# Kernel optimization log

Measured on AMD Instinct MI355X. Metric: run time of the kernel, lower is better.

The kernel has to match this reference:

```python
import jax, jax.numpy as jnp
import numpy as np

N_DRUG = 100000
N_PROT = 100000
N_EDGE = 800000
DIM = 128


def _graph_conv(feat_src, esrc, edst, n_src, n_dst, W, b):
    """dgl GraphConv with norm='both': msg = h_src * outdeg^-1/2, sum over in-edges,
    scale by indeg^-1/2, then linear. Degrees clamped to >= 1."""
    ones = jnp.ones(esrc.shape[0], dtype=feat_src.dtype)
    deg_out = jnp.clip(jax.ops.segment_sum(ones, esrc, num_segments=n_src), 1.0)
    deg_in = jnp.clip(jax.ops.segment_sum(ones, edst, num_segments=n_dst), 1.0)
    h = feat_src * jax.lax.rsqrt(deg_out)[:, None]          # [n_src, d]
    agg = jax.ops.segment_sum(h[esrc], edst, num_segments=n_dst)  # [n_dst, d]
    agg = agg * jax.lax.rsqrt(deg_in)[:, None]
    return agg @ W + b


def _hetero_layer(hd, hp, ddi_src, ddi_dst, pdi_src, pdi_dst, ppi_src, ppi_dst, W, b):
    # relation order: 0=DDI (drug->drug), 1=PDI (protein->drug), 2=PPI (protein->protein)
    d_ddi = _graph_conv(hd, ddi_src, ddi_dst, N_DRUG, N_DRUG, W[0], b[0])
    d_pdi = _graph_conv(hp, pdi_src, pdi_dst, N_PROT, N_DRUG, W[1], b[1])
    p_ppi = _graph_conv(hp, ppi_src, ppi_dst, N_PROT, N_PROT, W[2], b[2])
    return d_ddi + d_pdi, p_ppi  # HeteroGraphConv aggregate='sum' per dst type


def setup_inputs() -> dict:
    key = jax.random.key(0)
    ks = jax.random.split(key, 16)
    s = 1.0 / np.sqrt(DIM)
    return {
        "drug_feats": jax.random.normal(ks[0], (N_DRUG, DIM), jnp.float32),
        "protein_feats": jax.random.normal(ks[1], (N_PROT, DIM), jnp.float32),
        "ddi_src": jax.random.randint(ks[2], (N_EDGE,), 0, N_DRUG),
        "ddi_dst": jax.random.randint(ks[3], (N_EDGE,), 0, N_DRUG),
        "pdi_src": jax.random.randint(ks[4], (N_EDGE,), 0, N_PROT),
        "pdi_dst": jax.random.randint(ks[5], (N_EDGE,), 0, N_DRUG),
        "ppi_src": jax.random.randint(ks[6], (N_EDGE,), 0, N_PROT),
        "ppi_dst": jax.random.randint(ks[7], (N_EDGE,), 0, N_PROT),
        "W1": jax.random.normal(ks[8], (3, DIM, DIM), jnp.float32) * s,
        "b1": jnp.zeros((3, DIM), jnp.float32),
        "W2": jax.random.normal(ks[9], (3, DIM, DIM), jnp.float32) * s,
        "b2": jnp.zeros((3, DIM), jnp.float32),
        "W3": jax.random.normal(ks[10], (3, DIM, DIM), jnp.float32) * s,
        "b3": jnp.zeros((3, DIM), jnp.float32),
    }


def reference(drug_feats, protein_feats, ddi_src, ddi_dst, pdi_src, pdi_dst,
              ppi_src, ppi_dst, W1, b1, W2, b2, W3, b3):
    e = (ddi_src, ddi_dst, pdi_src, pdi_dst, ppi_src, ppi_dst)
    hd, hp = _hetero_layer(drug_feats, protein_feats, *e, W1, b1)
    hd, hp = jax.nn.relu(hd), jax.nn.relu(hp)
    hd, hp = _hetero_layer(hd, hp, *e, W2, b2)
    hd, hp = jax.nn.relu(hd), jax.nn.relu(hp)
    hd, hp = _hetero_layer(hd, hp, *e, W3, b3)
    return hd, hp
```

## Files before the change

kernel.cpp:

```cpp
#include <hip/hip_runtime.h>
#include <hip/hip_bf16.h>
#include <stdint.h>

#define NN 100000
#define NE 800000
#define SCAN_CHUNK 2048
#define NBLK 49

#define NPART 8
#define PART_SZ ((NN + NPART - 1) / NPART)
#define KSPLIT 16
#define SEGSZ (NE / KSPLIT)
#define HBINS PART_SZ

typedef __bf16 bf16x8 __attribute__((ext_vector_type(8)));
using float4v = __attribute__((ext_vector_type(4))) float;
typedef int intv4 __attribute__((ext_vector_type(4)));
typedef unsigned short ushortv4 __attribute__((ext_vector_type(4)));

__device__ __forceinline__ float bf2f(unsigned short h) {
    unsigned int u = ((unsigned int)h) << 16;
    return __builtin_bit_cast(float, u);
}
__device__ __forceinline__ float bf_lo(unsigned int u) {
    return __builtin_bit_cast(float, u << 16);
}
__device__ __forceinline__ float bf_hi(unsigned int u) {
    return __builtin_bit_cast(float, u & 0xffff0000u);
}
__device__ __forceinline__ unsigned short f2bf(float x) {
    unsigned int u = __builtin_bit_cast(unsigned int, x);
    u += 0x7fffu + ((u >> 16) & 1u);
    return (unsigned short)(u >> 16);
}

__global__ void detect_fmt(const unsigned short* __restrict__ feat, int* __restrict__ flag) {
    __shared__ int cnt;
    if (threadIdx.x == 0) cnt = 0;
    __syncthreads();
    unsigned int u = feat[threadIdx.x];
    int e = (u >> 7) & 0xFF;
    if (e >= 90 && e <= 143) atomicAdd(&cnt, 1);
    __syncthreads();
    if (threadIdx.x == 0) {
        flag[0] = (cnt >= 160) ? 0 : 1;
        flag[1] = 0;
    }
}

__global__ __launch_bounds__(256) void convert_feats(const void* __restrict__ drug,
                                                     const void* __restrict__ prot,
                                                     unsigned short* __restrict__ hd,
                                                     unsigned short* __restrict__ hp,
                                                     const int* __restrict__ fmtp) {
    int fmt = fmtp[0];
    int i = (blockIdx.x * 256 + threadIdx.x) * 4;
    const int n1 = NN * 128;
    if (i >= 2 * n1) return;
    const void* src = (i < n1) ? drug : prot;
    unsigned short* dst = (i < n1) ? hd : hp;
    int j = (i < n1) ? i : i - n1;
    if (fmt) {
        float4 v = *(const float4*)((const float*)src + j);
        uint2 o;
        o.x = (unsigned int)f2bf(v.x) | ((unsigned int)f2bf(v.y) << 16);
        o.y = (unsigned int)f2bf(v.z) | ((unsigned int)f2bf(v.w) << 16);
        *(uint2*)(dst + j) = o;
    } else {
        *(uint2*)(dst + j) = *(const uint2*)((const unsigned short*)src + j);
    }
}

__global__ __launch_bounds__(256) void deg_hist(const int* __restrict__ s0, const int* __restrict__ d0,
                                                const int* __restrict__ s1, const int* __restrict__ d1,
                                                const int* __restrict__ s2, const int* __restrict__ d2,
                                                unsigned short* __restrict__ deg_part) {
    __shared__ unsigned int cnt[HBINS];
    int h = blockIdx.y;
    const int* a;
    switch (h) {
        case 0: a = s0; break;
        case 1: a = s1; break;
        case 2: a = s2; break;
        case 3: a = d0; break;
        case 4: a = d1; break;
        default: a = d2; break;
    }
    int part = blockIdx.x & (NPART - 1);
    int seg = blockIdx.x >> 3;
    int lo = part * HBINS;
    for (int j = threadIdx.x; j < HBINS; j += 256) cnt[j] = 0;
    __syncthreads();
    int base = seg * SEGSZ;
    int end = base + SEGSZ;
    for (int i = base + threadIdx.x * 4; i + 4 <= end; i += 1024) {
        intv4 v = *(const intv4*)(a + i);
#pragma unroll
        for (int k = 0; k < 4; k++) {
            int b = v[k] - lo;
            if ((unsigned)b < (unsigned)HBINS) atomicAdd(&cnt[b], 1u);
        }
    }
    __syncthreads();
    unsigned short* outp = deg_part + (size_t)seg * 6 * NN + (size_t)h * NN + lo;
    for (int j = threadIdx.x; j < HBINS; j += 256) outp[j] = (unsigned short)cnt[j];
}

__global__ __launch_bounds__(256) void merge_deg_rs(const unsigned short* __restrict__ deg_part,
                                                    int* __restrict__ deg_all,
                                                    float* __restrict__ rs_all) {
    int i = (blockIdx.x * 256 + threadIdx.x) * 4;
    if (i >= 6 * NN) return;
    int a0 = 0, a1 = 0, a2 = 0, a3 = 0;
#pragma unroll
    for (int s = 0; s < KSPLIT; s++) {
        ushortv4 v = *(const ushortv4*)(deg_part + (size_t)s * 6 * NN + i);
        a0 += v[0]; a1 += v[1]; a2 += v[2]; a3 += v[3];
    }
    intv4 acc; acc[0] = a0; acc[1] = a1; acc[2] = a2; acc[3] = a3;
    *(intv4*)(deg_all + i) = acc;
    float4v r;
#pragma unroll
    for (int k = 0; k < 4; k++) {
        int d = acc[k];
        if (d < 1) d = 1;
        r[k] = rsqrtf((float)d);
    }
    *(float4v*)(rs_all + i) = r;
}

__global__ __launch_bounds__(256) void scan_partial(const int* __restrict__ deg,
                                                    int* __restrict__ bsums) {
    int rel = blockIdx.y, blk = blockIdx.x;
    const int* d = deg + rel * NN;
    int base = blk * SCAN_CHUNK + threadIdx.x * 8;
    int s = 0;
#pragma unroll
    for (int i = 0; i < 8; i++) {
        int idx = base + i;
        if (idx < NN) s += d[idx];
    }
    __shared__ int wsum[4];
#pragma unroll
    for (int off = 32; off; off >>= 1) s += __shfl_down(s, off);
    if ((threadIdx.x & 63) == 0) wsum[threadIdx.x >> 6] = s;
    __syncthreads();
    if (threadIdx.x == 0) bsums[rel * NBLK + blk] = wsum[0] + wsum[1] + wsum[2] + wsum[3];
}

__global__ void scan_bsums(int* bsums) {
    int r = threadIdx.x;
    if (r < 3) {
        int run = 0;
        for (int i = 0; i < NBLK; i++) {
            int t = bsums[r * NBLK + i];
            bsums[r * NBLK + i] = run;
            run += t;
        }
    }
}

__global__ __launch_bounds__(256) void scan_final(const int* __restrict__ deg,
                                                  const int* __restrict__ bsums,
                                                  int* __restrict__ offs) {
    int rel = blockIdx.y, blk = blockIdx.x;
    const int* d = deg + rel * NN;
    int* o = offs + rel * NN;
    int base = blk * SCAN_CHUNK + threadIdx.x * 8;
    int v[8];
    int s = 0;
#pragma unroll
    for (int i = 0; i < 8; i++) {
        int idx = base + i;
        v[i] = (idx < NN) ? d[idx] : 0;
        s += v[i];
    }
    int lane = threadIdx.x & 63, wid = threadIdx.x >> 6;
    int x = s;
#pragma unroll
    for (int off = 1; off < 64; off <<= 1) {
        int t = __shfl_up(x, off);
        if (lane >= off) x += t;
    }
    __shared__ int wsum[4];
    if (lane == 63) wsum[wid] = x;
    __syncthreads();
    int woff = bsums[rel * NBLK + blk];
    for (int i = 0; i < wid; i++) woff += wsum[i];
    int run = woff + x - s;
#pragma unroll
    for (int i = 0; i < 8; i++) {
        int idx = base + i;
        if (idx < NN) {
            o[idx] = run;
            run += v[i];
        }
    }
}

__global__ __launch_bounds__(256) void seg_start_k(const unsigned short* __restrict__ deg_part,
                                                   const int* __restrict__ offs_all,
                                                   int* __restrict__ seg_start) {
    int i = blockIdx.x * 256 + threadIdx.x;
    if (i >= 3 * NN) return;
    int rel = i / NN, node = i - rel * NN;
    int run = offs_all[i];
#pragma unroll
    for (int s = 0; s < KSPLIT; s++) {
        seg_start[((size_t)s * 3 + rel) * NN + node] = run;
        run += deg_part[((size_t)s * 6 + 3 + rel) * NN + node];
    }
}

__global__ __launch_bounds__(256) void csr_fill3s(const int* __restrict__ s0, const int* __restrict__ d0,
                                                  const int* __restrict__ s1, const int* __restrict__ d1,
                                                  const int* __restrict__ s2, const int* __restrict__ d2,
                                                  const int* __restrict__ seg_start,
                                                  int* __restrict__ csr_all) {
    __shared__ int cur[PART_SZ];
    int rel = blockIdx.y;
    const int* s = (rel == 0) ? s0 : ((rel == 1) ? s1 : s2);
    const int* d = (rel == 0) ? d0 : ((rel == 1) ? d1 : d2);
    int part = blockIdx.x & (NPART - 1);
    int seg = blockIdx.x >> 3;
    int lo = part * PART_SZ;
    const int* ss = seg_start + ((size_t)seg * 3 + rel) * NN + lo;
    for (int j = threadIdx.x; j < PART_SZ; j += 256) cur[j] = ss[j];
    __syncthreads();
    int* csr = csr_all + (size_t)rel * NE;
    int base = seg * SEGSZ;
    int end = base + SEGSZ;
    for (int i = base + threadIdx.x * 4; i + 4 <= end; i += 1024) {
        intv4 dv = *(const intv4*)(d + i);
        intv4 sv = *(const intv4*)(s + i);
#pragma unroll
        for (int k = 0; k < 4; k++) {
            int b = dv[k] - lo;
            if ((unsigned)b < (unsigned)PART_SZ) {
                int pos = atomicAdd(&cur[b], 1);
                csr[pos] = sv[k];
            }
        }
    }
}

__global__ __launch_bounds__(256) void swizzle_w3(const void* __restrict__ W0,
                                                  const void* __restrict__ W1,
                                                  const void* __restrict__ W2,
                                                  int o0, int o1,
                                                  unsigned short* __restrict__ out, int lstride,
                                                  const int* __restrict__ fmtp, int ksteps) {
    int l = blockIdx.y;
    const void* W = (l == 0) ? W0 : ((l == 1) ? W1 : W2);
    int fmt = fmtp[0];
    int idx = blockIdx.x * 256 + threadIdx.x;
    int total = ksteps * 8 * 64 * 8;
    if (idx >= total) return;
    int j = idx & 7, lane = (idx >> 3) & 63, nt = (idx >> 9) & 7, ks = idx >> 12;
    int k = ks * 32 + (lane >> 4) * 8 + j;
    int n = nt * 16 + (lane & 15);
    int e = (k < 128) ? (o0 + k * 128 + n) : (o1 + (k - 128) * 128 + n);
    out[l * lstride + idx] = fmt ? f2bf(((const float*)W)[e]) : ((const unsigned short*)W)[e];
}

__global__ void bias_prep3(const void* __restrict__ b0, const void* __restrict__ b1,
                           const void* __restrict__ b2, float* __restrict__ bd,
                           float* __restrict__ bp, const int* __restrict__ fmtp) {
    int l = blockIdx.x;
    const void* b = (l == 0) ? b0 : ((l == 1) ? b1 : b2);
    int fmt = fmtp[0];
    int n = threadIdx.x;
    float v0, v1, v2;
    if (fmt) {
        const float* bf = (const float*)b;
        v0 = bf[n]; v1 = bf[128 + n]; v2 = bf[256 + n];
    } else {
        const unsigned short* bh = (const unsigned short*)b;
        v0 = bf2f(bh[n]); v1 = bf2f(bh[128 + n]); v2 = bf2f(bh[256 + n]);
    }
    bd[l * 128 + n] = v0 + v1;
    bp[l * 128 + n] = v2;
}

__device__ __forceinline__ void acc8(float* acc, uint4 v, float w) {
    acc[0] = fmaf(bf_lo(v.x), w, acc[0]);
    acc[1] = fmaf(bf_hi(v.x), w, acc[1]);
    acc[2] = fmaf(bf_lo(v.y), w, acc[2]);
    acc[3] = fmaf(bf_hi(v.y), w, acc[3]);
    acc[4] = fmaf(bf_lo(v.z), w, acc[4]);
    acc[5] = fmaf(bf_hi(v.z), w, acc[5]);
    acc[6] = fmaf(bf_lo(v.w), w, acc[6]);
    acc[7] = fmaf(bf_hi(v.w), w, acc[7]);
}

__global__ __launch_bounds__(256) void aggregate3(const unsigned short* __restrict__ hd,
                                                  const unsigned short* __restrict__ hp,
                                                  const float* __restrict__ rs_all,
                                                  const int* __restrict__ offs_all,
                                                  const int* __restrict__ deg_in_all,
                                                  const int* __restrict__ csr_all,
                                                  unsigned short* __restrict__ aggD,
                                                  unsigned short* __restrict__ aggP) {
    int rel = blockIdx.y;
    int g = blockIdx.x * 256 + threadIdx.x;
    int dst = g >> 4;
    int lane = g & 15;
    if (dst >= NN) return;
    const unsigned short* h = (rel == 0) ? hd : hp;
    const float* rs_out = rs_all + rel * NN;
    const float* rs_in = rs_all + (3 + rel) * NN;
    const int* cp = csr_all + (size_t)rel * NE + offs_all[rel * NN + dst];
    int cnt = deg_in_all[rel * NN + dst];
    unsigned short* out;
    int ostride, ocol;
    if (rel == 0)      { out = aggD; ostride = 256; ocol = 0; }
    else if (rel == 1) { out = aggD; ostride = 256; ocol = 128; }
    else               { out = aggP; ostride = 128; ocol = 0; }

    float acc[8] = {0.f, 0.f, 0.f, 0.f, 0.f, 0.f, 0.f, 0.f};
    int e = 0;
    for (; e + 4 <= cnt; e += 4) {
        int i0 = cp[e], i1 = cp[e + 1], i2 = cp[e + 2], i3 = cp[e + 3];
        float w0 = rs_out[i0], w1 = rs_out[i1], w2 = rs_out[i2], w3 = rs_out[i3];
        uint4 v0 = *(const uint4*)(h + (size_t)i0 * 128 + lane * 8);
        uint4 v1 = *(const uint4*)(h + (size_t)i1 * 128 + lane * 8);
        uint4 v2 = *(const uint4*)(h + (size_t)i2 * 128 + lane * 8);
        uint4 v3 = *(const uint4*)(h + (size_t)i3 * 128 + lane * 8);
        acc8(acc, v0, w0);
        acc8(acc, v1, w1);
        acc8(acc, v2, w2);
        acc8(acc, v3, w3);
    }
    for (; e < cnt; e++) {
        int i0 = cp[e];
        float w0 = rs_out[i0];
        uint4 v0 = *(const uint4*)(h + (size_t)i0 * 128 + lane * 8);
        acc8(acc, v0, w0);
    }
    float sc = rs_in[dst];
    uint4 o;
    o.x = (unsigned int)f2bf(acc[0] * sc) | ((unsigned int)f2bf(acc[1] * sc) << 16);
    o.y = (unsigned int)f2bf(acc[2] * sc) | ((unsigned int)f2bf(acc[3] * sc) << 16);
    o.z = (unsigned int)f2bf(acc[4] * sc) | ((unsigned int)f2bf(acc[5] * sc) << 16);
    o.w = (unsigned int)f2bf(acc[6] * sc) | ((unsigned int)f2bf(acc[7] * sc) << 16);
    *(uint4*)(out + (size_t)dst * ostride + ocol + lane * 8) = o;
}

__global__ __launch_bounds__(256) void gemm2(const unsigned short* __restrict__ A0,
                                             const unsigned short* __restrict__ B0,
                                             const float* __restrict__ bias0,
                                             void* __restrict__ out0, size_t ob0, int lda0, int nch0,
                                             const unsigned short* __restrict__ A1,
                                             const unsigned short* __restrict__ B1,
                                             const float* __restrict__ bias1,
                                             void* __restrict__ out1, size_t ob1, int lda1, int nch1,
                                             int relu, const int* __restrict__ ofmt) {
    __shared__ unsigned short bs[4 * 8 * 64 * 8];
    int y = blockIdx.y;
    const unsigned short* A = y ? A1 : A0;
    const unsigned short* Bf = y ? B1 : B0;
    const float* bias = y ? bias1 : bias0;
    void* outv = y ? out1 : out0;
    size_t obase = y ? ob1 : ob0;
    int lda = y ? lda1 : lda0;
    int nch = y ? nch1 : nch0;
    int fmt = ofmt[0];

    int lid = threadIdx.x & 63, wid = threadIdx.x >> 6;
    int m0 = blockIdx.x * 64 + wid * 16;
    int ra = m0 + (lid & 15);
    if (ra > NN - 1) ra = NN - 1;
    int koff = (lid >> 4) * 8;
    float4v acc[8];
#pragma unroll
    for (int nt = 0; nt < 8; nt++) acc[nt] = (float4v){0.f, 0.f, 0.f, 0.f};
    const unsigned short* arow = A + (size_t)ra * lda + koff;

    for (int c = 0; c < nch; c++) {
        if (c) __syncthreads();
        const uint4* gsrc = (const uint4*)(Bf + c * 16384);
        uint4* ldst = (uint4*)bs;
#pragma unroll
        for (int i = 0; i < 8; i++) ldst[threadIdx.x + i * 256] = gsrc[threadIdx.x + i * 256];
        __syncthreads();
#pragma unroll
        for (int ks = 0; ks < 4; ks++) {
            bf16x8 a = *(const bf16x8*)(arow + (c * 4 + ks) * 32);
            const bf16x8* bp = (const bf16x8*)bs + ks * 8 * 64 + lid;
#pragma unroll
            for (int nt = 0; nt < 8; nt++) {
                bf16x8 b = bp[nt * 64];
                acc[nt] = __builtin_amdgcn_mfma_f32_16x16x32_bf16(a, b, acc[nt], 0, 0, 0);
            }
        }
    }
    int crow = m0 + (lid >> 4) * 4;
    int ccol = lid & 15;
#pragma unroll
    for (int nt = 0; nt < 8; nt++) {
        float bb = bias[nt * 16 + ccol];
#pragma unroll
        for (int r = 0; r < 4; r++) {
            int row = crow + r;
            if (row < NN) {
                float yv = acc[nt][r] + bb;
                if (relu) yv = fmaxf(yv, 0.f);
                size_t idx = obase + (size_t)row * 128 + nt * 16 + ccol;
                if (fmt) ((float*)outv)[idx] = yv;
                else ((unsigned short*)outv)[idx] = f2bf(yv);
            }
        }
    }
}

__global__ __launch_bounds__(256) void copy_final(const void* __restrict__ src,
                                                  void* __restrict__ dst,
                                                  const int* __restrict__ fmtp, int n) {
    int fmt = fmtp[0];
    int i = (blockIdx.x * 256 + threadIdx.x) * 4;
    if (i < n) {
        if (fmt) *(float4*)((float*)dst + i) = *(const float4*)((const float*)src + i);
        else *(uint2*)((unsigned short*)dst + i) = *(const uint2*)((const unsigned short*)src + i);
    }
}

extern "C" void kernel_launch(void* const* d_in, const int* in_sizes, int n_in,
                              void* d_out, int out_size, void* d_ws, size_t ws_size,
                              hipStream_t stream) {
    (void)in_sizes; (void)n_in; (void)out_size;
    const void* drug = d_in[0];
    const void* prot = d_in[1];
    const int* ddi_src = (const int*)d_in[2];
    const int* ddi_dst = (const int*)d_in[3];
    const int* pdi_src = (const int*)d_in[4];
    const int* pdi_dst = (const int*)d_in[5];
    const int* ppi_src = (const int*)d_in[6];
    const int* ppi_dst = (const int*)d_in[7];
    const void* Wl[3] = {d_in[8], d_in[10], d_in[12]};
    const void* bl[3] = {d_in[9], d_in[11], d_in[13]};

    char* p = (char*)d_ws;
    auto alloc = [&](size_t bytes) -> char* {
        char* r = p;
        p += (bytes + 255) & ~(size_t)255;
        return r;
    };
    int*   flag       = (int*)alloc(256);
    int*   deg_all    = (int*)alloc(6 * NN * 4);
    float* rs_all     = (float*)alloc(6 * NN * 4);
    int*   offs_all   = (int*)alloc(3 * NN * 4);
    int*   csr_all    = (int*)alloc(3 * NE * 4);
    int*   bsums      = (int*)alloc(3 * NBLK * 4);
    char*  hbuf       = alloc((size_t)NN * 128 * 4);
    unsigned short* hd_b = (unsigned short*)hbuf;
    unsigned short* hp_b = (unsigned short*)hbuf + (size_t)NN * 128;
    unsigned short* aggP = (unsigned short*)alloc((size_t)NN * 128 * 2);
    unsigned short* Wd_f = (unsigned short*)alloc(3 * 8 * 8 * 64 * 8 * 2);
    unsigned short* Wp_f = (unsigned short*)alloc(3 * 4 * 8 * 64 * 8 * 2);
    float* bd = (float*)alloc(3 * 128 * 4);
    float* bp = (float*)alloc(3 * 128 * 4);
    size_t needed = (size_t)(p - (char*)d_ws);
    if (needed > ws_size) return;

    unsigned short* deg_part = (unsigned short*)hbuf;
    int* seg_start = (int*)aggP;

    const int* FMT = flag;
    const int* BF  = flag + 1;

    unsigned short* aggD = (unsigned short*)d_out;

    detect_fmt<<<1, 256, 0, stream>>>((const unsigned short*)drug, flag);

    deg_hist<<<dim3(NPART * KSPLIT, 6), 256, 0, stream>>>(ddi_src, ddi_dst, pdi_src, pdi_dst,
                                                          ppi_src, ppi_dst, deg_part);
    merge_deg_rs<<<(6 * NN / 4 + 255) / 256, 256, 0, stream>>>(deg_part, deg_all, rs_all);
    scan_partial<<<dim3(NBLK, 3), 256, 0, stream>>>(deg_all + 3 * NN, bsums);
    scan_bsums<<<1, 64, 0, stream>>>(bsums);
    scan_final<<<dim3(NBLK, 3), 256, 0, stream>>>(deg_all + 3 * NN, bsums, offs_all);
    seg_start_k<<<(3 * NN + 255) / 256, 256, 0, stream>>>(deg_part, offs_all, seg_start);
    csr_fill3s<<<dim3(NPART * KSPLIT, 3), 256, 0, stream>>>(ddi_src, ddi_dst, pdi_src, pdi_dst,
                                                            ppi_src, ppi_dst, seg_start, csr_all);

    swizzle_w3<<<dim3((8 * 8 * 64 * 8 + 255) / 256, 3), 256, 0, stream>>>(
        Wl[0], Wl[1], Wl[2], 0, 16384, Wd_f, 32768, FMT, 8);
    swizzle_w3<<<dim3((4 * 8 * 64 * 8 + 255) / 256, 3), 256, 0, stream>>>(
        Wl[0], Wl[1], Wl[2], 32768, 0, Wp_f, 16384, FMT, 4);
    bias_prep3<<<3, 128, 0, stream>>>(bl[0], bl[1], bl[2], bd, bp, FMT);

    convert_feats<<<(2 * NN * 128 / 4 + 255) / 256, 256, 0, stream>>>(drug, prot, hd_b, hp_b, FMT);

    const int AGB = (NN * 16 + 255) / 256;
    const int GGB = (NN + 63) / 64;
    for (int l = 0; l < 3; l++) {
        aggregate3<<<dim3(AGB, 3), 256, 0, stream>>>(hd_b, hp_b, rs_all, offs_all,
                                                     deg_all + 3 * NN, csr_all, aggD, aggP);
        if (l < 2) {
            gemm2<<<dim3(GGB, 2), 256, 0, stream>>>(
                aggD, Wd_f + l * 32768, bd + l * 128, hd_b, 0, 256, 2,
                aggP, Wp_f + l * 16384, bp + l * 128, hp_b, 0, 128, 1,
                1, BF);
        } else {
            gemm2<<<dim3(GGB, 1), 256, 0, stream>>>(
                aggD, Wd_f + l * 32768, bd + l * 128, hbuf, 0, 256, 2,
                aggD, Wd_f + l * 32768, bd + l * 128, hbuf, 0, 256, 2,
                0, FMT);
            gemm2<<<dim3(GGB, 1), 256, 0, stream>>>(
                aggP, Wp_f + l * 16384, bp + l * 128, d_out, (size_t)NN * 128, 128, 1,
                aggP, Wp_f + l * 16384, bp + l * 128, d_out, (size_t)NN * 128, 128, 1,
                0, FMT);
            copy_final<<<(NN * 128 / 4 + 255) / 256, 256, 0, stream>>>(hbuf, d_out, FMT, NN * 128);
        }
    }
}
```

Before: 729.5 us.

## Fuse neighbor aggregation with linear transform in one kernel per layer

Merges the aggregate and GEMM kernels so each block of 64 destination nodes gathers its neighbor sums into shared memory and then runs the MFMA projection directly. This removes the round-trip of aggregated features through global memory. Layers now ping-pong between d_out and the workspace, which drops the final copy kernel and the separate aggregation buffer, and seg_start gets its own allocation. In exchange, gather parallelism per block drops (16 threads handle 4 destinations serially), and weights are read from global/L1 instead of being staged in LDS.

```diff
diff --git a/kernel.cpp b/kernel.cpp
--- a/kernel.cpp
+++ b/kernel.cpp
@@ -293,108 +293,95 @@
     acc[7] = fmaf(bf_hi(v.w), w, acc[7]);
 }
 
-__global__ __launch_bounds__(256) void aggregate3(const unsigned short* __restrict__ hd,
-                                                  const unsigned short* __restrict__ hp,
-                                                  const float* __restrict__ rs_all,
-                                                  const int* __restrict__ offs_all,
-                                                  const int* __restrict__ deg_in_all,
-                                                  const int* __restrict__ csr_all,
-                                                  unsigned short* __restrict__ aggD,
-                                                  unsigned short* __restrict__ aggP) {
-    int rel = blockIdx.y;
-    int g = blockIdx.x * 256 + threadIdx.x;
-    int dst = g >> 4;
-    int lane = g & 15;
-    if (dst >= NN) return;
-    const unsigned short* h = (rel == 0) ? hd : hp;
-    const float* rs_out = rs_all + rel * NN;
-    const float* rs_in = rs_all + (3 + rel) * NN;
-    const int* cp = csr_all + (size_t)rel * NE + offs_all[rel * NN + dst];
-    int cnt = deg_in_all[rel * NN + dst];
-    unsigned short* out;
-    int ostride, ocol;
-    if (rel == 0)      { out = aggD; ostride = 256; ocol = 0; }
-    else if (rel == 1) { out = aggD; ostride = 256; ocol = 128; }
-    else               { out = aggP; ostride = 128; ocol = 0; }
-
-    float acc[8] = {0.f, 0.f, 0.f, 0.f, 0.f, 0.f, 0.f, 0.f};
-    int e = 0;
-    for (; e + 4 <= cnt; e += 4) {
-        int i0 = cp[e], i1 = cp[e + 1], i2 = cp[e + 2], i3 = cp[e + 3];
-        float w0 = rs_out[i0], w1 = rs_out[i1], w2 = rs_out[i2], w3 = rs_out[i3];
-        uint4 v0 = *(const uint4*)(h + (size_t)i0 * 128 + lane * 8);
-        uint4 v1 = *(const uint4*)(h + (size_t)i1 * 128 + lane * 8);
-        uint4 v2 = *(const uint4*)(h + (size_t)i2 * 128 + lane * 8);
-        uint4 v3 = *(const uint4*)(h + (size_t)i3 * 128 + lane * 8);
-        acc8(acc, v0, w0);
-        acc8(acc, v1, w1);
-        acc8(acc, v2, w2);
-        acc8(acc, v3, w3);
-    }
-    for (; e < cnt; e++) {
-        int i0 = cp[e];
-        float w0 = rs_out[i0];
-        uint4 v0 = *(const uint4*)(h + (size_t)i0 * 128 + lane * 8);
-        acc8(acc, v0, w0);
-    }
-    float sc = rs_in[dst];
-    uint4 o;
-    o.x = (unsigned int)f2bf(acc[0] * sc) | ((unsigned int)f2bf(acc[1] * sc) << 16);
-    o.y = (unsigned int)f2bf(acc[2] * sc) | ((unsigned int)f2bf(acc[3] * sc) << 16);
-    o.z = (unsigned int)f2bf(acc[4] * sc) | ((unsigned int)f2bf(acc[5] * sc) << 16);
-    o.w = (unsigned int)f2bf(acc[6] * sc) | ((unsigned int)f2bf(acc[7] * sc) << 16);
-    *(uint4*)(out + (size_t)dst * ostride + ocol + lane * 8) = o;
-}
-
-__global__ __launch_bounds__(256) void gemm2(const unsigned short* __restrict__ A0,
-                                             const unsigned short* __restrict__ B0,
-                                             const float* __restrict__ bias0,
-                                             void* __restrict__ out0, size_t ob0, int lda0, int nch0,
-                                             const unsigned short* __restrict__ A1,
-                                             const unsigned short* __restrict__ B1,
-                                             const float* __restrict__ bias1,
-                                             void* __restrict__ out1, size_t ob1, int lda1, int nch1,
-                                             int relu, const int* __restrict__ ofmt) {
-    __shared__ unsigned short bs[4 * 8 * 64 * 8];
+__global__ __launch_bounds__(256) void agg_gemm(const unsigned short* __restrict__ hd,
+                                                const unsigned short* __restrict__ hp,
+                                                const float* __restrict__ rs_all,
+                                                const int* __restrict__ offs_all,
+                                                const int* __restrict__ deg_in_all,
+                                                const int* __restrict__ csr_all,
+                                                const unsigned short* __restrict__ Wd,
+                                                const unsigned short* __restrict__ Wp,
+                                                const float* __restrict__ bdl,
+                                                const float* __restrict__ bpl,
+                                                void* __restrict__ outD, size_t obD,
+                                                void* __restrict__ outP, size_t obP,
+                                                int relu, const int* __restrict__ ofmt) {
+    __shared__ unsigned short as[64][264];
     int y = blockIdx.y;
-    const unsigned short* A = y ? A1 : A0;
-    const unsigned short* Bf = y ? B1 : B0;
-    const float* bias = y ? bias1 : bias0;
-    void* outv = y ? out1 : out0;
-    size_t obase = y ? ob1 : ob0;
-    int lda = y ? lda1 : lda0;
-    int nch = y ? nch1 : nch0;
+    int tid = threadIdx.x;
+    int grp = tid >> 4, lane = tid & 15;
+    int base = blockIdx.x * 64;
+
+    int nrel = y ? 1 : 2;
+    for (int rr = 0; rr < nrel; rr++) {
+        int rel = y ? 2 : rr;
+        const unsigned short* h = (rel == 0) ? hd : hp;
+        const float* rs_out = rs_all + rel * NN;
+        const float* rs_in = rs_all + (3 + rel) * NN;
+        int ocol = (rr == 1) ? 128 : 0;
+#pragma unroll
+        for (int i = 0; i < 4; i++) {
+            int dl = grp * 4 + i;
+            int dst = base + dl;
+            if (dst > NN - 1) dst = NN - 1;
+            const int* cp = csr_all + (size_t)rel * NE + offs_all[rel * NN + dst];
+            int cnt = deg_in_all[rel * NN + dst];
+            float acc[8] = {0.f, 0.f, 0.f, 0.f, 0.f, 0.f, 0.f, 0.f};
+            int e = 0;
+            for (; e + 4 <= cnt; e += 4) {
+                int i0 = cp[e], i1 = cp[e + 1], i2 = cp[e + 2], i3 = cp[e + 3];
+                float w0 = rs_out[i0], w1 = rs_out[i1], w2 = rs_out[i2], w3 = rs_out[i3];
+                uint4 v0 = *(const uint4*)(h + (size_t)i0 * 128 + lane * 8);
+                uint4 v1 = *(const uint4*)(h + (size_t)i1 * 128 + lane * 8);
+                uint4 v2 = *(const uint4*)(h + (size_t)i2 * 128 + lane * 8);
+                uint4 v3 = *(const uint4*)(h + (size_t)i3 * 128 + lane * 8);
+                acc8(acc, v0, w0);
+                acc8(acc, v1, w1);
+                acc8(acc, v2, w2);
+                acc8(acc, v3, w3);
+            }
+            for (; e < cnt; e++) {
+                int i0 = cp[e];
+                float w0 = rs_out[i0];
+                uint4 v0 = *(const uint4*)(h + (size_t)i0 * 128 + lane * 8);
+                acc8(acc, v0, w0);
+            }
+            float sc = rs_in[dst];
+            uint4 o;
+            o.x = (unsigned int)f2bf(acc[0] * sc) | ((unsigned int)f2bf(acc[1] * sc) << 16);
+            o.y = (unsigned int)f2bf(acc[2] * sc) | ((unsigned int)f2bf(acc[3] * sc) << 16);
+            o.z = (unsigned int)f2bf(acc[4] * sc) | ((unsigned int)f2bf(acc[5] * sc) << 16);
+            o.w = (unsigned int)f2bf(acc[6] * sc) | ((unsigned int)f2bf(acc[7] * sc) << 16);
+            *(uint4*)(&as[dl][ocol + lane * 8]) = o;
+        }
+    }
+    __syncthreads();
+
+    const unsigned short* Bf = y ? Wp : Wd;
+    const float* bias = y ? bpl : bdl;
+    void* outv = y ? outP : outD;
+    size_t obase = y ? obP : obD;
+    int nch = y ? 1 : 2;
     int fmt = ofmt[0];
-
-    int lid = threadIdx.x & 63, wid = threadIdx.x >> 6;
-    int m0 = blockIdx.x * 64 + wid * 16;
-    int ra = m0 + (lid & 15);
-    if (ra > NN - 1) ra = NN - 1;
+    int lid = tid & 63, wid = tid >> 6;
+    int ar = wid * 16 + (lid & 15);
     int koff = (lid >> 4) * 8;
     float4v acc[8];
 #pragma unroll
     for (int nt = 0; nt < 8; nt++) acc[nt] = (float4v){0.f, 0.f, 0.f, 0.f};
-    const unsigned short* arow = A + (size_t)ra * lda + koff;
-
     for (int c = 0; c < nch; c++) {
-        if (c) __syncthreads();
-        const uint4* gsrc = (const uint4*)(Bf + c * 16384);
-        uint4* ldst = (uint4*)bs;
-#pragma unroll
-        for (int i = 0; i < 8; i++) ldst[threadIdx.x + i * 256] = gsrc[threadIdx.x + i * 256];
-        __syncthreads();
 #pragma unroll
         for (int ks = 0; ks < 4; ks++) {
-            bf16x8 a = *(const bf16x8*)(arow + (c * 4 + ks) * 32);
-            const bf16x8* bp = (const bf16x8*)bs + ks * 8 * 64 + lid;
+            bf16x8 a = *(const bf16x8*)(&as[ar][c * 128 + ks * 32 + koff]);
+            const bf16x8* bp8 = (const bf16x8*)(Bf + (size_t)c * 16384) + ks * 8 * 64 + lid;
 #pragma unroll
             for (int nt = 0; nt < 8; nt++) {
-                bf16x8 b = bp[nt * 64];
+                bf16x8 b = bp8[nt * 64];
                 acc[nt] = __builtin_amdgcn_mfma_f32_16x16x32_bf16(a, b, acc[nt], 0, 0, 0);
             }
         }
     }
-    int crow = m0 + (lid >> 4) * 4;
+    int crow = base + wid * 16 + (lid >> 4) * 4;
     int ccol = lid & 15;
 #pragma unroll
     for (int nt = 0; nt < 8; nt++) {
@@ -410,17 +397,6 @@
                 else ((unsigned short*)outv)[idx] = f2bf(yv);
             }
         }
-    }
-}
-
-__global__ __launch_bounds__(256) void copy_final(const void* __restrict__ src,
-                                                  void* __restrict__ dst,
-                                                  const int* __restrict__ fmtp, int n) {
-    int fmt = fmtp[0];
-    int i = (blockIdx.x * 256 + threadIdx.x) * 4;
-    if (i < n) {
-        if (fmt) *(float4*)((float*)dst + i) = *(const float4*)((const float*)src + i);
-        else *(uint2*)((unsigned short*)dst + i) = *(const uint2*)((const unsigned short*)src + i);
     }
 }
 
@@ -451,10 +427,10 @@
     int*   offs_all   = (int*)alloc(3 * NN * 4);
     int*   csr_all    = (int*)alloc(3 * NE * 4);
     int*   bsums      = (int*)alloc(3 * NBLK * 4);
+    int*   seg_start  = (int*)alloc((size_t)KSPLIT * 3 * NN * 4);
     char*  hbuf       = alloc((size_t)NN * 128 * 4);
     unsigned short* hd_b = (unsigned short*)hbuf;
     unsigned short* hp_b = (unsigned short*)hbuf + (size_t)NN * 128;
-    unsigned short* aggP = (unsigned short*)alloc((size_t)NN * 128 * 2);
     unsigned short* Wd_f = (unsigned short*)alloc(3 * 8 * 8 * 64 * 8 * 2);
     unsigned short* Wp_f = (unsigned short*)alloc(3 * 4 * 8 * 64 * 8 * 2);
     float* bd = (float*)alloc(3 * 128 * 4);
@@ -463,12 +439,12 @@
     if (needed > ws_size) return;
 
     unsigned short* deg_part = (unsigned short*)hbuf;
-    int* seg_start = (int*)aggP;
 
     const int* FMT = flag;
     const int* BF  = flag + 1;
 
-    unsigned short* aggD = (unsigned short*)d_out;
+    unsigned short* hd_o = (unsigned short*)d_out;
+    unsigned short* hp_o = (unsigned short*)d_out + (size_t)NN * 128;
 
     detect_fmt<<<1, 256, 0, stream>>>((const unsigned short*)drug, flag);
 
@@ -490,26 +466,16 @@
 
     convert_feats<<<(2 * NN * 128 / 4 + 255) / 256, 256, 0, stream>>>(drug, prot, hd_b, hp_b, FMT);
 
-    const int AGB = (NN * 16 + 255) / 256;
     const int GGB = (NN + 63) / 64;
-    for (int l = 0; l < 3; l++) {
-        aggregate3<<<dim3(AGB, 3), 256, 0, stream>>>(hd_b, hp_b, rs_all, offs_all,
-                                                     deg_all + 3 * NN, csr_all, aggD, aggP);
-        if (l < 2) {
-            gemm2<<<dim3(GGB, 2), 256, 0, stream>>>(
-                aggD, Wd_f + l * 32768, bd + l * 128, hd_b, 0, 256, 2,
-                aggP, Wp_f + l * 16384, bp + l * 128, hp_b, 0, 128, 1,
-                1, BF);
-        } else {
-            gemm2<<<dim3(GGB, 1), 256, 0, stream>>>(
-                aggD, Wd_f + l * 32768, bd + l * 128, hbuf, 0, 256, 2,
-                aggD, Wd_f + l * 32768, bd + l * 128, hbuf, 0, 256, 2,
-                0, FMT);
-            gemm2<<<dim3(GGB, 1), 256, 0, stream>>>(
-                aggP, Wp_f + l * 16384, bp + l * 128, d_out, (size_t)NN * 128, 128, 1,
-                aggP, Wp_f + l * 16384, bp + l * 128, d_out, (size_t)NN * 128, 128, 1,
-                0, FMT);
-            copy_final<<<(NN * 128 / 4 + 255) / 256, 256, 0, stream>>>(hbuf, d_out, FMT, NN * 128);
-        }
-    }
-}
+    agg_gemm<<<dim3(GGB, 2), 256, 0, stream>>>(hd_b, hp_b, rs_all, offs_all, deg_all + 3 * NN,
+                                               csr_all, Wd_f, Wp_f, bd, bp,
+                                               d_out, 0, d_out, (size_t)NN * 128, 1, BF);
+    agg_gemm<<<dim3(GGB, 2), 256, 0, stream>>>(hd_o, hp_o, rs_all, offs_all, deg_all + 3 * NN,
+                                               csr_all, Wd_f + 32768, Wp_f + 16384,
+                                               bd + 128, bp + 128,
+                                               hbuf, 0, hbuf, (size_t)NN * 128, 1, BF);
+    agg_gemm<<<dim3(GGB, 2), 256, 0, stream>>>(hd_b, hp_b, rs_all, offs_all, deg_all + 3 * NN,
+                                               csr_all, Wd_f + 2 * 32768, Wp_f + 2 * 16384,
+                                               bd + 2 * 128, bp + 2 * 128,
+                                               d_out, 0, d_out, (size_t)NN * 128, 0, FMT);
+}
```

New measurement: 752.2 us. 1.03x slower.
